# Kernel tuning notes

Hardware: AMD Instinct MI355X
Metric: run time of the kernel (lower is better)

## Reference

```python
import jax, jax.numpy as jnp
import numpy as np

N = 50000      # nodes
E = 800000     # edges (avg degree 16)
D_IN = 64
D_H = 64


def setup_inputs() -> dict:
    key = jax.random.key(0)
    k = jax.random.split(key, 4)
    x = jax.random.normal(k[0], (N, D_IN), dtype=jnp.float32)
    edge_index = jax.random.randint(k[1], (2, E), 0, N, dtype=jnp.int64)
    W1 = jax.random.normal(k[2], (D_IN, D_H), dtype=jnp.float32) * (1.0 / np.sqrt(D_IN))
    b1 = jnp.zeros((D_H,), dtype=jnp.float32)
    W2 = jax.random.normal(k[3], (D_H, 1), dtype=jnp.float32) * (1.0 / np.sqrt(D_H))
    b2 = jnp.zeros((1,), dtype=jnp.float32)
    return {"x": x, "edge_index": edge_index, "W1": W1, "b1": b1, "W2": W2, "b2": b2}


def gcn_conv(x, src, dst, W, b):
    """PyG-style GCNConv: linear -> symmetric-normalized scatter-aggregate + bias.
    src/dst already include self-loops."""
    n = x.shape[0]
    h = x @ W                                                   # [N, Dout]
    deg = jax.ops.segment_sum(jnp.ones_like(dst, dtype=h.dtype), dst, num_segments=n)
    dinv_sqrt = jnp.where(deg > 0, jax.lax.rsqrt(jnp.maximum(deg, 1e-12)), 0.0)
    norm = dinv_sqrt[src] * dinv_sqrt[dst]                       # [E+N]
    agg = jax.ops.segment_sum(h[src] * norm[:, None], dst, num_segments=n)
    return agg + b


def reference(x, edge_index, W1, b1, W2, b2):
    n = x.shape[0]
    loops = jnp.arange(n, dtype=edge_index.dtype)
    src = jnp.concatenate([edge_index[0], loops])                # add self-loops
    dst = jnp.concatenate([edge_index[1], loops])
    h = jax.nn.relu(gcn_conv(x, src, dst, W1, b1))               # [N, D_H]
    out = gcn_conv(h, src, dst, W2, b2)                          # [N, 1]
    return out.squeeze(-1)                                       # [N]
```

## Files before the change

### kernel.cpp

```cpp
#include <hip/hip_runtime.h>
#include <hip/hip_fp16.h>

#define D 64
#define PW2 128
#define PSH2 7
#define EPB 2048

__global__ __launch_bounds__(512) void k_hist(const int* __restrict__ dst, int E,
                                              int* __restrict__ counts, int NP) {
    extern __shared__ int lh[];
    int t = threadIdx.x, b = blockIdx.x;
    for (int i = t; i < NP; i += 512) lh[i] = 0;
    __syncthreads();
    int base = b * EPB;
#pragma unroll
    for (int k = 0; k < EPB / 512; ++k) {
        int e = base + k * 512 + t;
        if (e < E) atomicAdd(&lh[dst[e] >> PSH2], 1);
    }
    __syncthreads();
    for (int i = t; i < NP; i += 512) counts[(size_t)b * NP + i] = lh[i];
}

__global__ __launch_bounds__(512) void k_scanA(int* __restrict__ counts, int NB, int NP,
                                               int* __restrict__ bin_total) {
    __shared__ int sh[512];
    int t = threadIdx.x, bin = blockIdx.x;
    int v = (t < NB) ? counts[(size_t)t * NP + bin] : 0;
    sh[t] = v;
    __syncthreads();
    for (int off = 1; off < 512; off <<= 1) {
        int u = (t >= off) ? sh[t - off] : 0;
        __syncthreads();
        sh[t] += u;
        __syncthreads();
    }
    if (t < NB) counts[(size_t)t * NP + bin] = sh[t] - v;
    if (t == 511) bin_total[bin] = sh[511];
}

__global__ __launch_bounds__(512) void k_scatter(const int* __restrict__ src,
        const int* __restrict__ dst, int E, const int* __restrict__ counts,
        const int* __restrict__ bin_total, int NP, int* __restrict__ csr_e) {
    __shared__ int sh[512];
    __shared__ int bb[512];
    extern __shared__ int cur[];
    int t = threadIdx.x, b = blockIdx.x;
    int v = (t < NP) ? bin_total[t] : 0;
    sh[t] = v;
    __syncthreads();
    for (int off = 1; off < 512; off <<= 1) {
        int u = (t >= off) ? sh[t - off] : 0;
        __syncthreads();
        sh[t] += u;
        __syncthreads();
    }
    bb[t] = sh[t] - v;
    __syncthreads();
    for (int i = t; i < NP; i += 512)
        cur[i] = counts[(size_t)b * NP + i] + bb[i];
    __syncthreads();
    int base = b * EPB;
#pragma unroll
    for (int k = 0; k < EPB / 512; ++k) {
        int e = base + k * 512 + t;
        if (e < E) {
            int s = src[e], d = dst[e];
            int pos = atomicAdd(&cur[d >> PSH2], 1);
            csr_e[pos] = s | ((d & (PW2 - 1)) << 16);
        }
    }
}

__global__ __launch_bounds__(512) void k_sort2zw(const int* __restrict__ csr_e,
        const int* __restrict__ bin_total, int NP, int n,
        const float* __restrict__ x, const float* __restrict__ W1,
        int* __restrict__ csr_src, int* __restrict__ row_ptr,
        float* __restrict__ dinv, __half* __restrict__ zh) {
    __shared__ int sh[512];
    __shared__ int cnt[PW2];
    __shared__ int cursor[PW2];
    __shared__ float ldv[PW2];
    __shared__ float lrow[8][D];
    __shared__ int s_beg, s_end;
    int t = threadIdx.x, p = blockIdx.x;

    int bv = (t < NP) ? bin_total[t] : 0;
    sh[t] = bv;
    __syncthreads();
    for (int off = 1; off < 512; off <<= 1) {
        int u = (t >= off) ? sh[t - off] : 0;
        __syncthreads();
        sh[t] += u;
        __syncthreads();
    }
    if (t == p) { s_beg = sh[t] - bv; s_end = sh[t]; }
    if (t < PW2) cnt[t] = 0;
    __syncthreads();
    int beg = s_beg, end = s_end;

    for (int i = beg + t; i < end; i += 512) atomicAdd(&cnt[csr_e[i] >> 16], 1);
    __syncthreads();
    int val = (t < PW2) ? cnt[t] : 0;
    sh[t] = val;
    __syncthreads();
    for (int off = 1; off < 512; off <<= 1) {
        int u = (t >= off) ? sh[t - off] : 0;
        __syncthreads();
        sh[t] += u;
        __syncthreads();
    }
    int excl = sh[t] - val;
    if (t < PW2) {
        cursor[t] = beg + excl;
        int node = p * PW2 + t;
        float dv = rsqrtf((float)(val + 1));
        ldv[t] = dv;
        if (node <= n) {
            row_ptr[node] = beg + excl;
            if (node < n) dinv[node] = dv;
        }
    }
    __syncthreads();
    for (int i = beg + t; i < end; i += 512) {
        int e = csr_e[i];
        int q = atomicAdd(&cursor[e >> 16], 1);
        csr_src[q] = e & 0xFFFF;
    }

    int wave = t >> 6, lane = t & 63;
    float w1c[D];
#pragma unroll
    for (int d = 0; d < D; ++d) w1c[d] = W1[d * D + lane];
    int r0 = wave * 16;
    for (int k = 0; k < 16; ++k) {
        int r = r0 + k;
        int node = p * PW2 + r;
        if (node >= n) break;
        lrow[wave][lane] = x[(size_t)node * D + lane];
        __builtin_amdgcn_wave_barrier();
        float h = 0.0f;
#pragma unroll
        for (int db = 0; db < D; db += 4) {
            float4 rr = *(const float4*)&lrow[wave][db];
            h = fmaf(rr.x, w1c[db], h);
            h = fmaf(rr.y, w1c[db + 1], h);
            h = fmaf(rr.z, w1c[db + 2], h);
            h = fmaf(rr.w, w1c[db + 3], h);
        }
        zh[(size_t)node * D + lane] = __float2half(h * ldv[r]);
        __builtin_amdgcn_wave_barrier();
    }
}

__global__ __launch_bounds__(256) void k_gather(
        const __half2* __restrict__ zh, const float* __restrict__ dinv,
        const int* __restrict__ row_ptr, const int* __restrict__ csr_src,
        const float* __restrict__ b1, const float* __restrict__ W2,
        float* __restrict__ sd, int n) {
    int tid = threadIdx.x;
    int wave = tid >> 6, lane = tid & 63;
    int eg = lane >> 3, dg = lane & 7;
    int v = blockIdx.x * 4 + wave;
    if (v >= n) return;
    float dv = dinv[v];
    int beg = row_ptr[v], end = row_ptr[v + 1];

    float4 A = make_float4(0.f, 0.f, 0.f, 0.f);
    float4 B = make_float4(0.f, 0.f, 0.f, 0.f);
    float2 f;
#define ACC16(r)                                                        \
    {   __half2 h0 = *(__half2*)&(r).x, h1 = *(__half2*)&(r).y,         \
                h2 = *(__half2*)&(r).z, h3 = *(__half2*)&(r).w;         \
        f = __half22float2(h0); A.x += f.x; A.y += f.y;                 \
        f = __half22float2(h1); A.z += f.x; A.w += f.y;                 \
        f = __half22float2(h2); B.x += f.x; B.y += f.y;                 \
        f = __half22float2(h3); B.z += f.x; B.w += f.y; }

    if (eg == 0) {
        int4 r = *(const int4*)(zh + (size_t)v * 32 + dg * 4);
        ACC16(r);
    }
    int base = beg;
    for (; base + 16 <= end; base += 16) {
        int u0 = csr_src[base + eg];
        int u1 = csr_src[base + 8 + eg];
        int4 r0 = *(const int4*)(zh + (size_t)u0 * 32 + dg * 4);
        int4 r1 = *(const int4*)(zh + (size_t)u1 * 32 + dg * 4);
        ACC16(r0);
        ACC16(r1);
    }
    for (; base < end; base += 8) {
        int idx = base + eg;
        if (idx < end) {
            int u = csr_src[idx];
            int4 r = *(const int4*)(zh + (size_t)u * 32 + dg * 4);
            ACC16(r);
        }
    }
#undef ACC16
#pragma unroll
    for (int off = 8; off <= 32; off <<= 1) {
        A.x += __shfl_xor(A.x, off, 64); A.y += __shfl_xor(A.y, off, 64);
        A.z += __shfl_xor(A.z, off, 64); A.w += __shfl_xor(A.w, off, 64);
        B.x += __shfl_xor(B.x, off, 64); B.y += __shfl_xor(B.y, off, 64);
        B.z += __shfl_xor(B.z, off, 64); B.w += __shfl_xor(B.w, off, 64);
    }
    float4 b1a = *(const float4*)&b1[dg * 8];
    float4 b1b = *(const float4*)&b1[dg * 8 + 4];
    float4 w2a = *(const float4*)&W2[dg * 8];
    float4 w2b = *(const float4*)&W2[dg * 8 + 4];
    float part;
    part  = fmaxf(fmaf(dv, A.x, b1a.x), 0.f) * w2a.x;
    part += fmaxf(fmaf(dv, A.y, b1a.y), 0.f) * w2a.y;
    part += fmaxf(fmaf(dv, A.z, b1a.z), 0.f) * w2a.z;
    part += fmaxf(fmaf(dv, A.w, b1a.w), 0.f) * w2a.w;
    part += fmaxf(fmaf(dv, B.x, b1b.x), 0.f) * w2b.x;
    part += fmaxf(fmaf(dv, B.y, b1b.y), 0.f) * w2b.y;
    part += fmaxf(fmaf(dv, B.z, b1b.z), 0.f) * w2b.z;
    part += fmaxf(fmaf(dv, B.w, b1b.w), 0.f) * w2b.w;
    part += __shfl_xor(part, 1, 64);
    part += __shfl_xor(part, 2, 64);
    part += __shfl_xor(part, 4, 64);
    if (lane == 0) sd[v] = part * dv;
}

__global__ __launch_bounds__(256) void k_out(const float* __restrict__ sd,
        const float* __restrict__ dinv, const int* __restrict__ row_ptr,
        const int* __restrict__ csr_src, const float* __restrict__ b2,
        float* __restrict__ out, int n) {
    int t = blockIdx.x * blockDim.x + threadIdx.x;
    int v = t >> 3, r = t & 7;
    if (v >= n) return;
    int beg = row_ptr[v], end = row_ptr[v + 1];
    float a = (r == 0) ? sd[v] : 0.0f;
    for (int i = beg + r; i < end; i += 8) a += sd[csr_src[i]];
    a += __shfl_xor(a, 1, 64);
    a += __shfl_xor(a, 2, 64);
    a += __shfl_xor(a, 4, 64);
    if (r == 0) out[v] = b2[0] + a * dinv[v];
}

extern "C" void kernel_launch(void* const* d_in, const int* in_sizes, int n_in,
                              void* d_out, int out_size, void* d_ws, size_t ws_size,
                              hipStream_t stream) {
    const float* x  = (const float*)d_in[0];
    const int*   ei = (const int*)d_in[1];
    const float* W1 = (const float*)d_in[2];
    const float* b1 = (const float*)d_in[3];
    const float* W2 = (const float*)d_in[4];
    const float* b2 = (const float*)d_in[5];

    int n = in_sizes[0] / D;
    int E = in_sizes[1] / 2;
    const int* src = ei;
    const int* dst = ei + E;

    int NP = (n + PW2 - 1) / PW2;
    int NB = (E + EPB - 1) / EPB;

    char* ws = (char*)d_ws;
    auto take = [&](size_t bytes) {
        char* p = ws;
        ws += (bytes + 255) & ~(size_t)255;
        return p;
    };
    int*     counts    = (int*)take((size_t)NB * NP * sizeof(int));
    int*     bin_total = (int*)take((size_t)NP * sizeof(int));
    int*     csr_e     = (int*)take((size_t)E * sizeof(int));
    int*     csr_src   = (int*)take((size_t)E * sizeof(int));
    int*     row_ptr   = (int*)take((size_t)(n + 1) * sizeof(int));
    float*   dinv      = (float*)take((size_t)n * sizeof(float));
    float*   sd        = (float*)take((size_t)n * sizeof(float));
    __half*  zh        = (__half*)take((size_t)n * D * sizeof(__half));

    float* out = (float*)d_out;
    size_t ldsNP = (size_t)NP * sizeof(int);

    k_hist<<<NB, 512, ldsNP, stream>>>(dst, E, counts, NP);
    k_scanA<<<NP, 512, 0, stream>>>(counts, NB, NP, bin_total);
    k_scatter<<<NB, 512, ldsNP, stream>>>(src, dst, E, counts, bin_total, NP, csr_e);
    k_sort2zw<<<NP, 512, 0, stream>>>(csr_e, bin_total, NP, n, x, W1,
                                      csr_src, row_ptr, dinv, zh);

    k_gather<<<(n + 3) / 4, 256, 0, stream>>>((const __half2*)zh, dinv, row_ptr,
                                              csr_src, b1, W2, sd, n);
    k_out<<<((size_t)n * 8 + 255) / 256, 256, 0, stream>>>(sd, dinv, row_ptr, csr_src,
                                                           b2, out, n);
}
```

Measured before the change: 77.27 us.

## Use wave-shuffle block scans, vectorized edge loads, and wider output gather

Replaces the shared-memory Hillis-Steele scans in four kernels with a wave-level shuffle scan plus an 8-entry cross-wave combine, cutting barrier count sharply. The histogram and scatter kernels now load src/dst as int4 per thread instead of strided scalar loads. The final aggregation kernel uses 16 lanes per node instead of 8. The vector loads assume 16-byte alignment of the edge arrays, and the scatter kernel now only initializes cursors for up to 512 bins.

After: 74.99 us, median of 2. -3.0%, faster.

```diff
diff --git a/kernel.cpp b/kernel.cpp
--- a/kernel.cpp
+++ b/kernel.cpp
@@ -5,6 +5,30 @@
 #define PW2 128
 #define PSH2 7
 #define EPB 2048
+
+__device__ __forceinline__ int wave_iscan64(int v, int lane) {
+#pragma unroll
+    for (int off = 1; off < 64; off <<= 1) {
+        int u = __shfl_up(v, off, 64);
+        if (lane >= off) v += u;
+    }
+    return v;
+}
+
+__device__ __forceinline__ int block_iscan512(int v, int t, int* wsum) {
+    int lane = t & 63, wave = t >> 6;
+    __syncthreads();
+    int s = wave_iscan64(v, lane);
+    if (lane == 63) wsum[wave] = s;
+    __syncthreads();
+    if (wave == 0) {
+        int wv = (lane < 8) ? wsum[lane] : 0;
+        int ws = wave_iscan64(wv, lane);
+        if (lane < 8) wsum[lane] = ws - wv;
+    }
+    __syncthreads();
+    return s + wsum[wave];
+}
 
 __global__ __launch_bounds__(512) void k_hist(const int* __restrict__ dst, int E,
                                               int* __restrict__ counts, int NP) {
@@ -12,11 +36,16 @@
     int t = threadIdx.x, b = blockIdx.x;
     for (int i = t; i < NP; i += 512) lh[i] = 0;
     __syncthreads();
-    int base = b * EPB;
-#pragma unroll
-    for (int k = 0; k < EPB / 512; ++k) {
-        int e = base + k * 512 + t;
-        if (e < E) atomicAdd(&lh[dst[e] >> PSH2], 1);
+    int e = b * EPB + t * 4;
+    if (e + 3 < E) {
+        int4 d4 = *(const int4*)&dst[e];
+        atomicAdd(&lh[d4.x >> PSH2], 1);
+        atomicAdd(&lh[d4.y >> PSH2], 1);
+        atomicAdd(&lh[d4.z >> PSH2], 1);
+        atomicAdd(&lh[d4.w >> PSH2], 1);
+    } else {
+        for (int k = 0; k < 4; ++k)
+            if (e + k < E) atomicAdd(&lh[dst[e + k] >> PSH2], 1);
     }
     __syncthreads();
     for (int i = t; i < NP; i += 512) counts[(size_t)b * NP + i] = lh[i];
@@ -24,50 +53,43 @@
 
 __global__ __launch_bounds__(512) void k_scanA(int* __restrict__ counts, int NB, int NP,
                                                int* __restrict__ bin_total) {
-    __shared__ int sh[512];
+    __shared__ int wsum[8];
     int t = threadIdx.x, bin = blockIdx.x;
     int v = (t < NB) ? counts[(size_t)t * NP + bin] : 0;
-    sh[t] = v;
-    __syncthreads();
-    for (int off = 1; off < 512; off <<= 1) {
-        int u = (t >= off) ? sh[t - off] : 0;
-        __syncthreads();
-        sh[t] += u;
-        __syncthreads();
-    }
-    if (t < NB) counts[(size_t)t * NP + bin] = sh[t] - v;
-    if (t == 511) bin_total[bin] = sh[511];
+    int incl = block_iscan512(v, t, wsum);
+    if (t < NB) counts[(size_t)t * NP + bin] = incl - v;
+    if (t == 511) bin_total[bin] = incl;
 }
 
 __global__ __launch_bounds__(512) void k_scatter(const int* __restrict__ src,
         const int* __restrict__ dst, int E, const int* __restrict__ counts,
         const int* __restrict__ bin_total, int NP, int* __restrict__ csr_e) {
-    __shared__ int sh[512];
-    __shared__ int bb[512];
+    __shared__ int wsum[8];
     extern __shared__ int cur[];
     int t = threadIdx.x, b = blockIdx.x;
     int v = (t < NP) ? bin_total[t] : 0;
-    sh[t] = v;
-    __syncthreads();
-    for (int off = 1; off < 512; off <<= 1) {
-        int u = (t >= off) ? sh[t - off] : 0;
-        __syncthreads();
-        sh[t] += u;
-        __syncthreads();
-    }
-    bb[t] = sh[t] - v;
-    __syncthreads();
-    for (int i = t; i < NP; i += 512)
-        cur[i] = counts[(size_t)b * NP + i] + bb[i];
-    __syncthreads();
-    int base = b * EPB;
-#pragma unroll
-    for (int k = 0; k < EPB / 512; ++k) {
-        int e = base + k * 512 + t;
-        if (e < E) {
-            int s = src[e], d = dst[e];
-            int pos = atomicAdd(&cur[d >> PSH2], 1);
-            csr_e[pos] = s | ((d & (PW2 - 1)) << 16);
+    int incl = block_iscan512(v, t, wsum);
+    if (t < NP) cur[t] = counts[(size_t)b * NP + t] + (incl - v);
+    __syncthreads();
+    int e = b * EPB + t * 4;
+    if (e + 3 < E) {
+        int4 s4 = *(const int4*)&src[e];
+        int4 d4 = *(const int4*)&dst[e];
+        int p0 = atomicAdd(&cur[d4.x >> PSH2], 1);
+        csr_e[p0] = s4.x | ((d4.x & (PW2 - 1)) << 16);
+        int p1 = atomicAdd(&cur[d4.y >> PSH2], 1);
+        csr_e[p1] = s4.y | ((d4.y & (PW2 - 1)) << 16);
+        int p2 = atomicAdd(&cur[d4.z >> PSH2], 1);
+        csr_e[p2] = s4.z | ((d4.z & (PW2 - 1)) << 16);
+        int p3 = atomicAdd(&cur[d4.w >> PSH2], 1);
+        csr_e[p3] = s4.w | ((d4.w & (PW2 - 1)) << 16);
+    } else {
+        for (int k = 0; k < 4; ++k) {
+            if (e + k < E) {
+                int s = src[e + k], d = dst[e + k];
+                int pos = atomicAdd(&cur[d >> PSH2], 1);
+                csr_e[pos] = s | ((d & (PW2 - 1)) << 16);
+            }
         }
     }
 }
@@ -77,7 +99,7 @@
         const float* __restrict__ x, const float* __restrict__ W1,
         int* __restrict__ csr_src, int* __restrict__ row_ptr,
         float* __restrict__ dinv, __half* __restrict__ zh) {
-    __shared__ int sh[512];
+    __shared__ int wsum[8];
     __shared__ int cnt[PW2];
     __shared__ int cursor[PW2];
     __shared__ float ldv[PW2];
@@ -86,15 +108,8 @@
     int t = threadIdx.x, p = blockIdx.x;
 
     int bv = (t < NP) ? bin_total[t] : 0;
-    sh[t] = bv;
-    __syncthreads();
-    for (int off = 1; off < 512; off <<= 1) {
-        int u = (t >= off) ? sh[t - off] : 0;
-        __syncthreads();
-        sh[t] += u;
-        __syncthreads();
-    }
-    if (t == p) { s_beg = sh[t] - bv; s_end = sh[t]; }
+    int incl = block_iscan512(bv, t, wsum);
+    if (t == p) { s_beg = incl - bv; s_end = incl; }
     if (t < PW2) cnt[t] = 0;
     __syncthreads();
     int beg = s_beg, end = s_end;
@@ -102,15 +117,8 @@
     for (int i = beg + t; i < end; i += 512) atomicAdd(&cnt[csr_e[i] >> 16], 1);
     __syncthreads();
     int val = (t < PW2) ? cnt[t] : 0;
-    sh[t] = val;
-    __syncthreads();
-    for (int off = 1; off < 512; off <<= 1) {
-        int u = (t >= off) ? sh[t - off] : 0;
-        __syncthreads();
-        sh[t] += u;
-        __syncthreads();
-    }
-    int excl = sh[t] - val;
+    int incl2 = block_iscan512(val, t, wsum);
+    int excl = incl2 - val;
     if (t < PW2) {
         cursor[t] = beg + excl;
         int node = p * PW2 + t;
@@ -230,14 +238,15 @@
         const int* __restrict__ csr_src, const float* __restrict__ b2,
         float* __restrict__ out, int n) {
     int t = blockIdx.x * blockDim.x + threadIdx.x;
-    int v = t >> 3, r = t & 7;
+    int v = t >> 4, r = t & 15;
     if (v >= n) return;
     int beg = row_ptr[v], end = row_ptr[v + 1];
     float a = (r == 0) ? sd[v] : 0.0f;
-    for (int i = beg + r; i < end; i += 8) a += sd[csr_src[i]];
+    for (int i = beg + r; i < end; i += 16) a += sd[csr_src[i]];
     a += __shfl_xor(a, 1, 64);
     a += __shfl_xor(a, 2, 64);
     a += __shfl_xor(a, 4, 64);
+    a += __shfl_xor(a, 8, 64);
     if (r == 0) out[v] = b2[0] + a * dinv[v];
 }
 
@@ -285,6 +294,6 @@
 
     k_gather<<<(n + 3) / 4, 256, 0, stream>>>((const __half2*)zh, dinv, row_ptr,
                                               csr_src, b1, W2, sd, n);
-    k_out<<<((size_t)n * 8 + 255) / 256, 256, 0, stream>>>(sd, dinv, row_ptr, csr_src,
-                                                           b2, out, n);
-}
+    k_out<<<((size_t)n * 16 + 255) / 256, 256, 0, stream>>>(sd, dinv, row_ptr, csr_src,
+                                                            b2, out, n);
+}
```
